# Kernel optimization log

Hardware: AMD Instinct MI355X
Metric: run time of the kernel (lower is better)

Reference implementation:

```python
import jax, jax.numpy as jnp
import numpy as np

K = 3  # kernel_dim
PAD = 1


def setup_inputs() -> dict:
    key = jax.random.key(0)
    ks = jax.random.split(key, 7)
    B, C_in, C_out, R = 2, 32, 64, 64
    H = W = D = 64
    return {
        "x": jax.random.normal(ks[0], (B, C_in, H, W, D), dtype=jnp.float32),
        "U_k_h": jax.random.normal(ks[1], (K, R), dtype=jnp.float32),
        "U_k_w": jax.random.normal(ks[2], (K, R), dtype=jnp.float32),
        "U_k_d": jax.random.normal(ks[3], (K, R), dtype=jnp.float32),
        "U_c_in": jax.random.normal(ks[4], (C_in, R), dtype=jnp.float32),
        "U_c_out": jax.random.normal(ks[5], (R, C_out), dtype=jnp.float32),
        "bias": jax.random.normal(ks[6], (C_out,), dtype=jnp.float32),
    }


def _cpd_conv3d(x, U_k_h, U_k_w, U_k_d, U_c_in, U_c_out, bias):
    # Equivalent to: patches[b,c,h,w,d,kh,kw,kd] contracted with
    # U_c_in[c,r] U_k_h[kh,r] U_k_w[kw,r] U_k_d[kd,r] U_c_out[r,co]
    # -> out[b,co,h,w,d].  We exploit the CP (rank-separable) structure
    # instead of materializing the unfolded patch tensor.
    xp = jnp.pad(x, ((0, 0), (0, 0), (PAD, PAD), (PAD, PAD), (PAD, PAD)))
    # channel contraction: [B, R, H+2, W+2, D+2]
    t = jnp.einsum('bchwd,cr->brhwd', xp, U_c_in)
    B, R, Hp, Wp, Dp = t.shape
    H, W, D = Hp - 2 * PAD, Wp - 2 * PAD, Dp - 2 * PAD
    # separable kernel contractions (fixed K=3 unrolled loops)
    t = sum(t[:, :, k:k + H, :, :] * U_k_h[k][None, :, None, None, None] for k in range(K))
    t = sum(t[:, :, :, k:k + W, :] * U_k_w[k][None, :, None, None, None] for k in range(K))
    t = sum(t[:, :, :, :, k:k + D] * U_k_d[k][None, :, None, None, None] for k in range(K))
    out = jnp.einsum('brhwd,rc->bchwd', t, U_c_out)
    return out + bias[None, :, None, None, None]


def reference(x, U_k_h, U_k_w, U_k_d, U_c_in, U_c_out, bias):
    return _cpd_conv3d(x, U_k_h, U_k_w, U_k_d, U_c_in, U_c_out, bias)
```

## Files before the change

kernel.cpp:

```cpp
#include <hip/hip_runtime.h>
#include <hip/hip_bf16.h>

typedef __attribute__((ext_vector_type(8))) short short8;
typedef __attribute__((ext_vector_type(4))) float f32x4;

__device__ __forceinline__ float b2f(short s) {
    return __uint_as_float(((unsigned int)(unsigned short)s) << 16);
}
__device__ __forceinline__ short f2b(float f) {
    unsigned int u = __float_as_uint(f);
    u += 0x7fffu + ((u >> 16) & 1u);
    return (short)(u >> 16);
}
__device__ __forceinline__ unsigned pack2(float a, float b) {
    return (unsigned)(unsigned short)f2b(a) | ((unsigned)(unsigned short)f2b(b) << 16);
}

__global__ __launch_bounds__(64)
void k0_prep(const float* __restrict__ Uco, short* __restrict__ ucotT)
{
    const int i  = blockIdx.x * 64 + threadIdx.x;
    const int co = i >> 6, r = i & 63;
    ucotT[co * 64 + r] = f2b(Uco[r * 64 + co]);
}

__global__ __launch_bounds__(256)
void k1_channel(const float* __restrict__ x,
                const float* __restrict__ Ucin,
                short* __restrict__ t)
{
    __shared__ float xs[128 * 36];
    const int tid  = threadIdx.x;
    const int bid  = blockIdx.x;
    const int b    = bid >> 11;
    const int sp0  = (bid & 2047) << 7;
    const float* xb = x + ((long)b << 23) + sp0;

    const int lane = tid & 63;
    const int wv   = tid >> 6;

    float u[32];
#pragma unroll
    for (int c = 0; c < 32; ++c) u[c] = Ucin[c * 64 + lane];

    for (int i = tid; i < 2048; i += 256) {
        int c2 = i >> 7;
        int so = i & 127;
        float a0 = xb[((long)(2 * c2)     << 18) + so];
        float a1 = xb[((long)(2 * c2 + 1) << 18) + so];
        float2 v; v.x = a0; v.y = a1;
        *(float2*)&xs[so * 36 + 2 * c2] = v;
    }
    __syncthreads();

    short* tb = t + (((size_t)b << 18) + sp0) * 64 + lane;
    for (int s = 0; s < 32; ++s) {
        const int so = wv * 32 + s;
        const float4* row = (const float4*)&xs[so * 36];
        float a0 = 0.f, a1 = 0.f;
#pragma unroll
        for (int k = 0; k < 8; ++k) {
            float4 xx = row[k];
            a0 += xx.x * u[4 * k + 0];
            a1 += xx.y * u[4 * k + 1];
            a0 += xx.z * u[4 * k + 2];
            a1 += xx.w * u[4 * k + 3];
        }
        tb[(size_t)so * 64] = f2b(a0 + a1);
    }
}

__global__ __launch_bounds__(256)
void k2_conv_gemm(const short* __restrict__ t,
                  const float* __restrict__ Ukh,
                  const float* __restrict__ Ukw,
                  const float* __restrict__ Ukd,
                  const float* __restrict__ Uco,
                  const float* __restrict__ bias,
                  const short* __restrict__ ucotT,
                  float* __restrict__ out)
{
    __shared__ short s[66 * 64];
    __shared__ short p[64 * 72];
    __shared__ short ucot[64 * 72];

    const int tid = threadIdx.x;

    const int bid  = blockIdx.x;
    const int slot = bid & 7;
    const int idx  = bid >> 3;
    const int b    = idx >> 9;
    const int rem  = idx & 511;
    const int h    = slot * 8 + (rem >> 6);
    const int w    = rem & 63;

    const short* colp[9];
    bool valid[9];
#pragma unroll
    for (int kh = 0; kh < 3; ++kh) {
#pragma unroll
        for (int kw = 0; kw < 3; ++kw) {
            int hh = h + kh - 1, ww = w + kw - 1;
            bool v = ((unsigned)hh < 64u) && ((unsigned)ww < 64u);
            valid[kh * 3 + kw] = v;
            long base = v ? ((long)(b * 262144 + hh * 4096 + ww * 64) << 6) : 0;
            colp[kh * 3 + kw] = t + base;
        }
    }

    if (ucotT) {
        for (int i = tid; i < 512; i += 256) {
            int co = i >> 3, rb = i & 7;
            short8 v = *(const short8*)&ucotT[co * 64 + rb * 8];
            *(short8*)&ucot[co * 72 + rb * 8] = v;
        }
    } else {
        for (int i = tid; i < 4096; i += 256) {
            int r = i >> 6, co = i & 63;
            ucot[co * 72 + r] = f2b(Uco[i]);
        }
    }

    const int rq = tid & 15;
    float4 W[9];
    {
        float4 a[3], c[3];
#pragma unroll
        for (int k = 0; k < 3; ++k) {
            a[k] = *(const float4*)&Ukh[k * 64 + 4 * rq];
            c[k] = *(const float4*)&Ukw[k * 64 + 4 * rq];
        }
#pragma unroll
        for (int kh = 0; kh < 3; ++kh)
#pragma unroll
            for (int kw = 0; kw < 3; ++kw) {
                int kk = kh * 3 + kw;
                float m = valid[kk] ? 1.f : 0.f;
                W[kk].x = a[kh].x * c[kw].x * m;
                W[kk].y = a[kh].y * c[kw].y * m;
                W[kk].z = a[kh].z * c[kw].z * m;
                W[kk].w = a[kh].w * c[kw].w * m;
            }
    }

    if (tid < 32) {
        int sd = (tid < 16) ? 0 : 65;
        int rr = tid & 15;
        uint2 z; z.x = 0u; z.y = 0u;
        *(uint2*)&s[sd * 64 + 4 * rr] = z;
    }

    {
        const int off0 = (tid >> 4) * 64 + 4 * rq;
        uint2 cur[9];
#pragma unroll
        for (int kk = 0; kk < 9; ++kk)
            cur[kk] = *(const uint2*)(colp[kk] + off0);

#pragma unroll
        for (int j = 0; j < 4; ++j) {
            uint2 nxt[9];
            if (j < 3) {
#pragma unroll
                for (int kk = 0; kk < 9; ++kk)
                    nxt[kk] = *(const uint2*)(colp[kk] + off0 + 1024 * (j + 1));
            }
            float a0 = 0.f, a1 = 0.f, a2 = 0.f, a3 = 0.f;
#pragma unroll
            for (int kk = 0; kk < 9; ++kk) {
                uint2 uu = cur[kk];
                a0 += W[kk].x * b2f((short)(uu.x));
                a1 += W[kk].y * b2f((short)(uu.x >> 16));
                a2 += W[kk].z * b2f((short)(uu.y));
                a3 += W[kk].w * b2f((short)(uu.y >> 16));
            }
            int sd = 1 + (tid >> 4) + 16 * j;
            uint2 o; o.x = pack2(a0, a1); o.y = pack2(a2, a3);
            *(uint2*)&s[sd * 64 + 4 * rq] = o;
            if (j < 3) {
#pragma unroll
                for (int kk = 0; kk < 9; ++kk) cur[kk] = nxt[kk];
            }
        }
    }
    __syncthreads();

    {
        float4 Wd[3];
#pragma unroll
        for (int k = 0; k < 3; ++k)
            Wd[k] = *(const float4*)&Ukd[k * 64 + 4 * rq];
        for (int u = tid; u < 64 * 16; u += 256) {
            int d = u >> 4;
            float a0 = 0.f, a1 = 0.f, a2 = 0.f, a3 = 0.f;
#pragma unroll
            for (int k = 0; k < 3; ++k) {
                uint2 uu = *(const uint2*)&s[(d + k) * 64 + 4 * rq];
                a0 += Wd[k].x * b2f((short)(uu.x));
                a1 += Wd[k].y * b2f((short)(uu.x >> 16));
                a2 += Wd[k].z * b2f((short)(uu.y));
                a3 += Wd[k].w * b2f((short)(uu.y >> 16));
            }
            uint2 o; o.x = pack2(a0, a1); o.y = pack2(a2, a3);
            *(uint2*)&p[d * 72 + 4 * rq] = o;
        }
    }
    __syncthreads();

    {
        const int lane = tid & 63, wv = tid >> 6;
        const int l15 = lane & 15, quad = lane >> 4;
        short8 afr0 = *(const short8*)&p[(wv * 16 + l15) * 72 + quad * 8];
        short8 afr1 = *(const short8*)&p[(wv * 16 + l15) * 72 + 32 + quad * 8];
        f32x4 acc[4] = {};
#pragma unroll
        for (int nt = 0; nt < 4; ++nt) {
            short8 b0 = *(const short8*)&ucot[(nt * 16 + l15) * 72 + quad * 8];
            short8 b1 = *(const short8*)&ucot[(nt * 16 + l15) * 72 + 32 + quad * 8];
            acc[nt] = __builtin_amdgcn_mfma_f32_16x16x32_bf16(afr0, b0, acc[nt], 0, 0, 0);
            acc[nt] = __builtin_amdgcn_mfma_f32_16x16x32_bf16(afr1, b1, acc[nt], 0, 0, 0);
        }
#pragma unroll
        for (int nt = 0; nt < 4; ++nt) {
            int co = nt * 16 + l15;
            float bs = bias[co];
            int d = wv * 16 + quad * 4;
            float4 o;
            o.x = acc[nt][0] + bs; o.y = acc[nt][1] + bs;
            o.z = acc[nt][2] + bs; o.w = acc[nt][3] + bs;
            long addr = ((long)(b * 64 + co) << 18) + (h << 12) + (w << 6) + d;
            *(float4*)&out[addr] = o;
        }
    }
}

#define NTH 512
#define NPADP 656
#define SMEM_BYTES ((NPADP*32 + NPADP*32 + 432*32 + 64*32 + 64*64)*2 + 576*4)

__global__ __launch_bounds__(NTH)
void cpd_conv3d_fused_fb(const float* __restrict__ x,
                         const float* __restrict__ Ukh,
                         const float* __restrict__ Ukw,
                         const float* __restrict__ Ukd,
                         const float* __restrict__ Ucin,
                         const float* __restrict__ Uco,
                         const float* __restrict__ bias,
                         float* __restrict__ out)
{
    extern __shared__ char smem[];
    short* xs   = (short*)smem;
    short* t0   = xs   + NPADP*32;
    short* t1   = t0   + NPADP*32;
    short* uct  = t1   + 432*32;
    short* ucot = uct  + 64*32;
    float* ukf  = (float*)(ucot + 64*64);

    const int tid  = threadIdx.x;
    const int lane = tid & 63;
    const int wv   = tid >> 6;
    const int l15  = lane & 15;
    const int quad = lane >> 4;
    const int rg   = tid & 3;

    const int bid = blockIdx.x;
    const int dt = bid & 3, wt = (bid >> 2) & 15, ht = (bid >> 6) & 15, b = bid >> 10;
    const int h0 = ht * 4, w0 = wt * 4, d0 = dt * 16;

    for (int i = tid; i < 576; i += NTH) {
        float v = (i < 192) ? Ukh[i] : (i < 384 ? Ukw[i - 192] : Ukd[i - 384]);
        ukf[i] = v;
    }
    for (int i = tid; i < 2048; i += NTH) {
        int r = i >> 5, c = i & 31;
        uct[i] = f2b(Ucin[c * 64 + r]);
    }
    for (int i = tid; i < 4096; i += NTH) {
        int co = i >> 6, r = i & 63;
        ucot[i] = f2b(Uco[r * 64 + co]);
    }
    for (int i = tid; i < NPADP * 32; i += NTH) {
        int pp = i >> 5, c = i & 31;
        float v = 0.f;
        if (pp < 648) {
            int ph = pp / 108, rem = pp - ph * 108;
            int pw = rem / 18, pd = rem - pw * 18;
            int gh = h0 + ph - 1, gw = w0 + pw - 1, gd = d0 + pd - 1;
            if ((unsigned)gh < 64u && (unsigned)gw < 64u && (unsigned)gd < 64u)
                v = x[((long)(b * 32 + c) << 18) + (gh << 12) + (gw << 6) + gd];
        }
        xs[i] = f2b(v);
    }
    __syncthreads();

    f32x4 acc[8] = {};

    for (int pass = 0; pass < 2; ++pass) {
        const int rbase = pass * 32;
        {
            const int nt = wv & 1;
            short8 bfrag = *(const short8*)&uct[(rbase + nt * 16 + l15) * 32 + quad * 8];
            for (int mt = (wv >> 1); mt <= 40; mt += 4) {
                short8 afrag = *(const short8*)&xs[(mt * 16 + l15) * 32 + quad * 8];
                f32x4 c = {};
                c = __builtin_amdgcn_mfma_f32_16x16x32_bf16(afrag, bfrag, c, 0, 0, 0);
                const int col = nt * 16 + l15;
#pragma unroll
                for (int i2 = 0; i2 < 4; ++i2)
                    t0[(mt * 16 + quad * 4 + i2) * 32 + col] = f2b(c[i2]);
            }
        }
        __syncthreads();
        {
            float wh[3][8];
#pragma unroll
            for (int k = 0; k < 3; ++k) {
                const float4* pp_ = (const float4*)&ukf[k * 64 + rbase + rg * 8];
                float4 u0 = pp_[0], u1 = pp_[1];
                wh[k][0]=u0.x; wh[k][1]=u0.y; wh[k][2]=u0.z; wh[k][3]=u0.w;
                wh[k][4]=u1.x; wh[k][5]=u1.y; wh[k][6]=u1.z; wh[k][7]=u1.w;
            }
            for (int item = tid; item < 1728; item += NTH) {
                int q = item >> 2;
                float v[8] = {};
#pragma unroll
                for (int k = 0; k < 3; ++k) {
                    short8 sv = *(const short8*)&t0[(q + k * 108) * 32 + rg * 8];
#pragma unroll
                    for (int j = 0; j < 8; ++j) v[j] += wh[k][j] * b2f(sv[j]);
                }
                short8 o;
#pragma unroll
                for (int j = 0; j < 8; ++j) o[j] = f2b(v[j]);
                *(short8*)&t1[q * 32 + rg * 8] = o;
            }
        }
        __syncthreads();
        {
            float ww[3][8];
#pragma unroll
            for (int k = 0; k < 3; ++k) {
                const float4* pp_ = (const float4*)&ukf[(3 + k) * 64 + rbase + rg * 8];
                float4 u0 = pp_[0], u1 = pp_[1];
                ww[k][0]=u0.x; ww[k][1]=u0.y; ww[k][2]=u0.z; ww[k][3]=u0.w;
                ww[k][4]=u1.x; ww[k][5]=u1.y; ww[k][6]=u1.z; ww[k][7]=u1.w;
            }
            for (int item = tid; item < 1152; item += NTH) {
                int q2 = item >> 2;
                int oh = q2 / 72;
                int src = q2 + oh * 36;
                float v[8] = {};
#pragma unroll
                for (int k = 0; k < 3; ++k) {
                    short8 sv = *(const short8*)&t1[(src + k * 18) * 32 + rg * 8];
#pragma unroll
                    for (int j = 0; j < 8; ++j) v[j] += ww[k][j] * b2f(sv[j]);
                }
                short8 o;
#pragma unroll
                for (int j = 0; j < 8; ++j) o[j] = f2b(v[j]);
                *(short8*)&t0[q2 * 32 + rg * 8] = o;
            }
        }
        __syncthreads();
        {
            float wd[3][8];
#pragma unroll
            for (int k = 0; k < 3; ++k) {
                const float4* pp_ = (const float4*)&ukf[(6 + k) * 64 + rbase + rg * 8];
                float4 u0 = pp_[0], u1 = pp_[1];
                wd[k][0]=u0.x; wd[k][1]=u0.y; wd[k][2]=u0.z; wd[k][3]=u0.w;
                wd[k][4]=u1.x; wd[k][5]=u1.y; wd[k][6]=u1.z; wd[k][7]=u1.w;
            }
            for (int item = tid; item < 1024; item += NTH) {
                int pq = item >> 2;
                int src = pq + (pq >> 4) * 2;
                float v[8] = {};
#pragma unroll
                for (int k = 0; k < 3; ++k) {
                    short8 sv = *(const short8*)&t0[(src + k) * 32 + rg * 8];
#pragma unroll
                    for (int j = 0; j < 8; ++j) v[j] += wd[k][j] * b2f(sv[j]);
                }
                short8 o;
#pragma unroll
                for (int j = 0; j < 8; ++j) o[j] = f2b(v[j]);
                *(short8*)&t1[pq * 32 + rg * 8] = o;
            }
        }
        __syncthreads();
        {
            short8 bfr[4];
#pragma unroll
            for (int nt = 0; nt < 4; ++nt)
                bfr[nt] = *(const short8*)&ucot[(nt * 16 + l15) * 64 + rbase + quad * 8];
#pragma unroll
            for (int i = 0; i < 8; ++i) {
                int mt = wv * 2 + (i >> 2), nt = i & 3;
                short8 afr = *(const short8*)&t1[(mt * 16 + l15) * 32 + quad * 8];
                acc[i] = __builtin_amdgcn_mfma_f32_16x16x32_bf16(afr, bfr[nt], acc[i], 0, 0, 0);
            }
        }
    }

#pragma unroll
    for (int i = 0; i < 8; ++i) {
        int mt = wv * 2 + (i >> 2), nt = i & 3;
        int co = nt * 16 + l15;
        int oh = mt >> 2, ow = mt & 3;
        float bs = bias[co];
        float4 o4;
        o4.x = acc[i][0] + bs; o4.y = acc[i][1] + bs;
        o4.z = acc[i][2] + bs; o4.w = acc[i][3] + bs;
        long addr = ((long)(b * 64 + co) << 18) + ((long)(h0 + oh) << 12)
                  + ((w0 + ow) << 6) + (d0 + quad * 4);
        *(float4*)&out[addr] = o4;
    }
}

extern "C" void kernel_launch(void* const* d_in, const int* in_sizes, int n_in,
                              void* d_out, int out_size, void* d_ws, size_t ws_size,
                              hipStream_t stream) {
    const float* x    = (const float*)d_in[0];
    const float* Ukh  = (const float*)d_in[1];
    const float* Ukw  = (const float*)d_in[2];
    const float* Ukd  = (const float*)d_in[3];
    const float* Ucin = (const float*)d_in[4];
    const float* Uco  = (const float*)d_in[5];
    const float* bias = (const float*)d_in[6];
    float* out = (float*)d_out;

    const size_t needT = (size_t)2 * 262144 * 64 * 2;
    const size_t needM = 4096 * 2;
    if (ws_size >= needT) {
        short* t = (short*)d_ws;
        short* ucotT = nullptr;
        if (ws_size >= needT + needM) {
            ucotT = (short*)((char*)d_ws + needT);
            k0_prep<<<64, 64, 0, stream>>>(Uco, ucotT);
        }
        k1_channel<<<4096, 256, 0, stream>>>(x, Ucin, t);
        k2_conv_gemm<<<8192, 256, 0, stream>>>(t, Ukh, Ukw, Ukd, Uco, bias, ucotT, out);
    } else {
        (void)hipFuncSetAttribute((const void*)cpd_conv3d_fused_fb,
                                  hipFuncAttributeMaxDynamicSharedMemorySize,
                                  SMEM_BYTES);
        cpd_conv3d_fused_fb<<<2048, NTH, SMEM_BYTES, stream>>>(
            x, Ukh, Ukw, Ukd, Ucin, Uco, bias, out);
    }
}
```

Before: 277.2 us.

## Use bf16 MFMA for channel contraction with pre-transposed Ucin in k1

```diff
diff --git a/kernel.cpp b/kernel.cpp
--- a/kernel.cpp
+++ b/kernel.cpp
@@ -17,56 +17,90 @@
 }
 
 __global__ __launch_bounds__(64)
-void k0_prep(const float* __restrict__ Uco, short* __restrict__ ucotT)
+void k0_prep(const float* __restrict__ Uco, const float* __restrict__ Ucin,
+             short* __restrict__ ucotT, short* __restrict__ ucinT)
 {
-    const int i  = blockIdx.x * 64 + threadIdx.x;
-    const int co = i >> 6, r = i & 63;
-    ucotT[co * 64 + r] = f2b(Uco[r * 64 + co]);
+    const int i = blockIdx.x * 64 + threadIdx.x;
+    if (i < 4096) {
+        int co = i >> 6, r = i & 63;
+        ucotT[co * 64 + r] = f2b(Uco[r * 64 + co]);
+    } else {
+        int j = i - 4096;
+        int r = j >> 5, c = j & 31;
+        ucinT[r * 32 + c] = f2b(Ucin[c * 64 + r]);
+    }
 }
 
 __global__ __launch_bounds__(256)
 void k1_channel(const float* __restrict__ x,
                 const float* __restrict__ Ucin,
+                const short* __restrict__ ucinT_g,
                 short* __restrict__ t)
 {
-    __shared__ float xs[128 * 36];
-    const int tid  = threadIdx.x;
-    const int bid  = blockIdx.x;
-    const int b    = bid >> 11;
-    const int sp0  = (bid & 2047) << 7;
-    const float* xb = x + ((long)b << 23) + sp0;
-
-    const int lane = tid & 63;
-    const int wv   = tid >> 6;
-
-    float u[32];
-#pragma unroll
-    for (int c = 0; c < 32; ++c) u[c] = Ucin[c * 64 + lane];
-
-    for (int i = tid; i < 2048; i += 256) {
-        int c2 = i >> 7;
-        int so = i & 127;
-        float a0 = xb[((long)(2 * c2)     << 18) + so];
-        float a1 = xb[((long)(2 * c2 + 1) << 18) + so];
-        float2 v; v.x = a0; v.y = a1;
-        *(float2*)&xs[so * 36 + 2 * c2] = v;
+    __shared__ short xs[256 * 32];
+    __shared__ short uci[64 * 32];
+
+    const int tid = threadIdx.x;
+    const int gp0 = blockIdx.x * 256;
+    const int b   = gp0 >> 18;
+    const int sp  = (gp0 & 262143) + tid;
+    const float* xp = x + ((long)b << 23) + sp;
+
+    if (ucinT_g) {
+        ((short8*)uci)[tid] = ((const short8*)ucinT_g)[tid];
+    } else {
+        for (int i = tid; i < 2048; i += 256) {
+            int r = i >> 5, c = i & 31;
+            uci[i] = f2b(Ucin[c * 64 + r]);
+        }
+    }
+
+    {
+        float v[32];
+#pragma unroll
+        for (int c = 0; c < 32; ++c) v[c] = xp[(long)c << 18];
+        const int swz = (tid >> 1) & 3;
+#pragma unroll
+        for (int oct = 0; oct < 4; ++oct) {
+            short8 o;
+#pragma unroll
+            for (int j = 0; j < 8; ++j) o[j] = f2b(v[oct * 8 + j]);
+            *(short8*)&xs[tid * 32 + ((oct ^ swz) << 3)] = o;
+        }
     }
     __syncthreads();
 
-    short* tb = t + (((size_t)b << 18) + sp0) * 64 + lane;
-    for (int s = 0; s < 32; ++s) {
-        const int so = wv * 32 + s;
-        const float4* row = (const float4*)&xs[so * 36];
-        float a0 = 0.f, a1 = 0.f;
-#pragma unroll
-        for (int k = 0; k < 8; ++k) {
-            float4 xx = row[k];
-            a0 += xx.x * u[4 * k + 0];
-            a1 += xx.y * u[4 * k + 1];
-            a0 += xx.z * u[4 * k + 2];
-            a1 += xx.w * u[4 * k + 3];
-        }
-        tb[(size_t)so * 64] = f2b(a0 + a1);
+    const int lane = tid & 63, wv = tid >> 6;
+    const int l15 = lane & 15, quad = lane >> 4;
+
+    short8 afr[4];
+#pragma unroll
+    for (int mt = 0; mt < 4; ++mt)
+        afr[mt] = *(const short8*)&uci[(mt * 16 + l15) * 32 + quad * 8];
+
+    f32x4 acc[4][4] = {};
+#pragma unroll
+    for (int nt = 0; nt < 4; ++nt) {
+        const int srow = wv * 64 + nt * 16 + l15;
+        const int slot = quad ^ ((srow >> 1) & 3);
+        short8 bfr = *(const short8*)&xs[srow * 32 + (slot << 3)];
+#pragma unroll
+        for (int mt = 0; mt < 4; ++mt)
+            acc[mt][nt] = __builtin_amdgcn_mfma_f32_16x16x32_bf16(
+                afr[mt], bfr, acc[mt][nt], 0, 0, 0);
+    }
+
+#pragma unroll
+    for (int nt = 0; nt < 4; ++nt) {
+        const int srow = wv * 64 + nt * 16 + l15;
+        short* tb = t + ((size_t)(gp0 + srow) << 6);
+#pragma unroll
+        for (int mt = 0; mt < 4; ++mt) {
+            uint2 o;
+            o.x = pack2(acc[mt][nt][0], acc[mt][nt][1]);
+            o.y = pack2(acc[mt][nt][2], acc[mt][nt][3]);
+            *(uint2*)&tb[mt * 16 + quad * 4] = o;
+        }
     }
 }
 
@@ -431,15 +465,17 @@
     float* out = (float*)d_out;
 
     const size_t needT = (size_t)2 * 262144 * 64 * 2;
-    const size_t needM = 4096 * 2;
+    const size_t needM = (4096 + 2048) * 2;
     if (ws_size >= needT) {
         short* t = (short*)d_ws;
         short* ucotT = nullptr;
+        short* ucinT = nullptr;
         if (ws_size >= needT + needM) {
             ucotT = (short*)((char*)d_ws + needT);
-            k0_prep<<<64, 64, 0, stream>>>(Uco, ucotT);
-        }
-        k1_channel<<<4096, 256, 0, stream>>>(x, Ucin, t);
+            ucinT = ucotT + 4096;
+            k0_prep<<<96, 64, 0, stream>>>(Uco, Ucin, ucotT, ucinT);
+        }
+        k1_channel<<<2048, 256, 0, stream>>>(x, Ucin, ucinT, t);
         k2_conv_gemm<<<8192, 256, 0, stream>>>(t, Ukh, Ukw, Ukd, Uco, bias, ucotT, out);
     } else {
         (void)hipFuncSetAttribute((const void*)cpd_conv3d_fused_fb,
```

Result: faster. 264.3 us (-4.6%).
